# Performance work log

Hardware: AMD Instinct MI355X
Metric: run time of the kernel (lower is better)

Reference implementation:

```python
import jax, jax.numpy as jnp
import numpy as np

S_, T_, F_, SF_, G_ = 16, 400, 16, 250, 4  # systems, time, features, shuffleFactor, feature groups


def setup_inputs() -> dict:
    key = jax.random.key(0)
    ks = jax.random.split(key, 10)
    observations = jax.random.normal(ks[0], (S_, T_, F_), dtype=jnp.float32)
    mu = 0.1 * jax.random.normal(ks[1], (F_, 1), dtype=jnp.float32)
    Sigma_minus_half = (0.1 * jax.random.normal(ks[2], (F_, F_), dtype=jnp.float32)
                        + jnp.eye(F_, dtype=jnp.float32))
    # true random permutations of the time axis, per (shuffle-rep, feature-group, system)
    perm_idx = jnp.argsort(jax.random.uniform(ks[3], (SF_, G_, S_, T_)), axis=-1).astype(jnp.int32)
    W1 = jax.random.normal(ks[4], (F_, 32), dtype=jnp.float32) / jnp.sqrt(F_)
    b1 = jnp.zeros((32,), jnp.float32)
    W2 = jax.random.normal(ks[5], (32, 16), dtype=jnp.float32) / jnp.sqrt(32.0)
    b2 = jnp.zeros((16,), jnp.float32)
    W3 = jax.random.normal(ks[6], (16, 1), dtype=jnp.float32) / 4.0
    b3 = jnp.zeros((1,), jnp.float32)
    return dict(observations=observations, mu=mu, Sigma_minus_half=Sigma_minus_half,
                perm_idx=perm_idx, W1=W1, b1=b1, W2=W2, b2=b2, W3=W3, b3=b3)


def reference(observations, mu, Sigma_minus_half, perm_idx, W1, b1, W2, b2, W3, b3):
    # --- multipleShuffles: per-system, per-feature-group time permutation, repeated SF_ times ---
    feat_group = jnp.repeat(jnp.arange(G_), F_ // G_)          # [F] feature -> group id
    p = perm_idx[:, feat_group]                                 # [SF, F, S, T]
    p = jnp.transpose(p, (2, 0, 3, 1)).astype(jnp.int32)        # [S, SF, T, F]
    shuf = jnp.take_along_axis(observations[:, None, :, :], p, axis=2)  # [S, SF, T, F]
    shuf = shuf.reshape(S_, SF_ * T_, F_)                       # [S, SF*T, F]

    # --- normalizeObservations: Sigma^{-1/2} @ (z - mu) applied per (system, time) ---
    def normalize(x):
        return jnp.einsum('ij,stj->sti', Sigma_minus_half, x - mu[:, 0])

    # --- sequence MLP: Linear(F,32)-LeakyReLU-Linear(32,16)-LeakyReLU-Linear(16,1)-Sigmoid ---
    def mlp(x):
        h = jax.nn.leaky_relu(x @ W1 + b1, negative_slope=0.01)
        h = jax.nn.leaky_relu(h @ W2 + b2, negative_slope=0.01)
        return jax.nn.sigmoid(h @ W3 + b3)

    comb = mlp(normalize(observations))      # [S, T, 1]
    comb_shuf = mlp(normalize(shuf))         # [S, SF*T, 1]
    return jnp.concatenate([comb, comb_shuf], axis=1)  # [S, T*(1+SF), 1]
```

## Files before the change

### kernel.cpp

```cpp
#include <hip/hip_runtime.h>
#include <hip/hip_fp16.h>

#define S_N 16
#define T_N 400
#define F_N 16
#define SF_N 250
#define G_N 4
#define OUT_ROW 100400

typedef _Float16 f16x8 __attribute__((ext_vector_type(8)));
typedef float    f32x4 __attribute__((ext_vector_type(4)));

union QU { uint4 u; f16x8 v; };

#define QTAB_OFF   0
#define W2FRAG_OFF 1638400
#define B1H_OFF    1639424
#define B2F_OFF    1639488
#define W3F_OFF    1639552
#define B3F_OFF    1639616

#define LDS_U4     8000

__global__ __launch_bounds__(64) void precompute_kernel(
    const float* __restrict__ obs,
    const float* __restrict__ mu,
    const float* __restrict__ Sig,
    const float* __restrict__ W1,
    const float* __restrict__ b1,
    const float* __restrict__ W2,
    const float* __restrict__ b2,
    const float* __restrict__ W3,
    const float* __restrict__ b3,
    __half* __restrict__ qtab,
    __half* __restrict__ w2frag,
    __half* __restrict__ b1h,
    float* __restrict__ b2f,
    float* __restrict__ w3f,
    float* __restrict__ b3f,
    float* __restrict__ out)
{
    __shared__ float sAm[512];
    __shared__ float sW2[512];
    __shared__ float sMu[16];
    __shared__ float sB1[32];
    __shared__ float sB2[16];
    __shared__ float sW3[16];
    __shared__ float sB3;

    const int tid = threadIdx.x;

    for (int e = tid; e < 512; e += 64) {
        int j = e >> 5, k = e & 31;
        float acc = 0.f;
        #pragma unroll
        for (int i = 0; i < 16; ++i)
            acc = fmaf(Sig[i * 16 + j], W1[i * 32 + k], acc);
        sAm[e] = acc;
        sW2[e] = W2[e];
    }
    if (tid < 16) sMu[tid] = mu[tid];
    if (tid < 32) sB1[tid] = b1[tid];
    if (tid < 16) sB2[tid] = b2[tid];
    if (tid < 16) sW3[tid] = W3[tid];
    if (tid == 0) sB3 = b3[0];
    __syncthreads();

    if (blockIdx.x == 0) {
        {
            int n = tid & 15, cc = tid >> 4;
            #pragma unroll
            for (int j = 0; j < 8; ++j)
                w2frag[tid * 8 + j] = __float2half(sW2[(cc * 8 + j) * 16 + n]);
        }
        if (tid < 32) b1h[tid] = __float2half(sB1[tid]);
        if (tid < 16) b2f[tid] = sB2[tid];
        if (tid < 16) w3f[tid] = sW3[tid];
        if (tid == 0) b3f[0] = sB3;
    }

    const int gid = blockIdx.x * 64 + tid;
    const int s = gid / T_N;
    const int t = gid - s * T_N;

    float xm[16];
    {
        const float4* op = (const float4*)(obs + (size_t)gid * 16);
        float4 o0 = op[0], o1 = op[1], o2 = op[2], o3 = op[3];
        float v[16] = {o0.x, o0.y, o0.z, o0.w, o1.x, o1.y, o1.z, o1.w,
                       o2.x, o2.y, o2.z, o2.w, o3.x, o3.y, o3.z, o3.w};
        #pragma unroll
        for (int j = 0; j < 16; ++j) xm[j] = v[j] - sMu[j];
    }

    float h1[32];
    #pragma unroll
    for (int k = 0; k < 32; ++k) h1[k] = sB1[k];

    #pragma unroll
    for (int g = 0; g < 4; ++g) {
        float qg[32];
        #pragma unroll
        for (int k = 0; k < 32; ++k) {
            float a = xm[4 * g + 0] * sAm[(4 * g + 0) * 32 + k];
            a = fmaf(xm[4 * g + 1], sAm[(4 * g + 1) * 32 + k], a);
            a = fmaf(xm[4 * g + 2], sAm[(4 * g + 2) * 32 + k], a);
            a = fmaf(xm[4 * g + 3], sAm[(4 * g + 3) * 32 + k], a);
            qg[k] = a;
            h1[k] += a;
        }
        __half2* dst = (__half2*)(qtab + ((size_t)(s * 4 + g) * T_N + t) * 32);
        #pragma unroll
        for (int k2 = 0; k2 < 16; ++k2)
            dst[k2] = __floats2half2_rn(qg[2 * k2], qg[2 * k2 + 1]);
    }

    #pragma unroll
    for (int k = 0; k < 32; ++k) h1[k] = fmaxf(h1[k], 0.01f * h1[k]);

    float h2[16];
    #pragma unroll
    for (int j = 0; j < 16; ++j) h2[j] = sB2[j];
    #pragma unroll
    for (int k = 0; k < 32; ++k) {
        float a = h1[k];
        #pragma unroll
        for (int j = 0; j < 16; ++j) h2[j] = fmaf(a, sW2[k * 16 + j], h2[j]);
    }
    float acc = sB3;
    #pragma unroll
    for (int j = 0; j < 16; ++j) {
        float hj = fmaxf(h2[j], 0.01f * h2[j]);
        acc = fmaf(hj, sW3[j], acc);
    }
    out[(size_t)s * OUT_ROW + t] = 1.f / (1.f + __expf(-acc));
}

__global__ __launch_bounds__(1024, 4) void eval_kernel(
    const int* __restrict__ perm,
    const __half* __restrict__ qtab,
    const __half* __restrict__ w2frag,
    const __half* __restrict__ b1h,
    const float* __restrict__ b2f,
    const float* __restrict__ w3f,
    const float* __restrict__ b3p,
    float* __restrict__ out)
{
    extern __shared__ uint4 smem[];

    const int tid   = threadIdx.x;
    const int s     = blockIdx.x >> 4;
    const int chunk = blockIdx.x & 15;
    const int j0b   = chunk * 6250;

    const uint4* qsrc = (const uint4*)(qtab + (size_t)s * 1600 * 32);
    for (int e = tid; e < 6400; e += 1024) {
        int r = e >> 2, cc = e & 3;
        smem[r * 5 + cc] = qsrc[e];
    }
    __syncthreads();

    const int lane = tid & 63;
    const int wv   = tid >> 6;
    const int m    = lane & 15;
    const int c    = lane >> 4;

    const f16x8 afrag = *(const f16x8*)(w2frag + lane * 8);
    const f16x8 b1v   = *(const f16x8*)(b1h + c * 8);
    const float4 b2v  = *(const float4*)(b2f + c * 4);
    const float4 w3v  = *(const float4*)(w3f + c * 4);
    const float  b3   = b3p[0];

    for (int tile = wv; tile < 98; tile += 16) {
        const int jt = j0b + tile * 64;

        int idx[4][4];
        #pragma unroll
        for (int q = 0; q < 4; ++q) {
            int j = jt + q * 16 + m;
            int jc = j0b + 6249;
            if (j < jc) jc = j;
            const int sf = jc / 400;
            const int t  = jc - sf * 400;
            const int pb = sf * 25600 + s * 400 + t;
            #pragma unroll
            for (int g = 0; g < 4; ++g)
                idx[q][g] = perm[pb + g * 6400];
        }

        float res0, res1, res2, res3;
        #pragma unroll
        for (int q = 0; q < 4; ++q) {
            QU a0, a1, a2, a3;
            a0.u = smem[(idx[q][0]         ) * 5 + c];
            a1.u = smem[( 400 + idx[q][1]  ) * 5 + c];
            a2.u = smem[( 800 + idx[q][2]  ) * 5 + c];
            a3.u = smem[(1200 + idx[q][3]  ) * 5 + c];

            f16x8 h = (a0.v + a1.v) + (a2.v + a3.v) + b1v;
            #pragma unroll
            for (int k = 0; k < 8; ++k) {
                _Float16 x = h[k];
                _Float16 y = x * (_Float16)0.01f;
                h[k] = x > y ? x : y;
            }

            f32x4 acc = {0.f, 0.f, 0.f, 0.f};
            acc = __builtin_amdgcn_mfma_f32_16x16x32_f16(afrag, h, acc, 0, 0, 0);

            float p;
            {
                float v0 = acc[0] + b2v.x; v0 = fmaxf(v0, 0.01f * v0); p = v0 * w3v.x;
                float v1 = acc[1] + b2v.y; v1 = fmaxf(v1, 0.01f * v1); p = fmaf(v1, w3v.y, p);
                float v2 = acc[2] + b2v.z; v2 = fmaxf(v2, 0.01f * v2); p = fmaf(v2, w3v.z, p);
                float v3 = acc[3] + b2v.w; v3 = fmaxf(v3, 0.01f * v3); p = fmaf(v3, w3v.w, p);
            }
            p += __shfl_xor(p, 16);
            p += __shfl_xor(p, 32);
            if (q == 0) res0 = p;
            else if (q == 1) res1 = p;
            else if (q == 2) res2 = p;
            else res3 = p;
        }

        float v = res0;
        if (c == 1) v = res1;
        if (c == 2) v = res2;
        if (c == 3) v = res3;
        v += b3;
        const float sg = 1.f / (1.f + __expf(-v));
        const int j = jt + lane;
        if (j < j0b + 6250)
            out[(size_t)s * OUT_ROW + 400 + j] = sg;
    }
}

extern "C" void kernel_launch(void* const* d_in, const int* in_sizes, int n_in,
                              void* d_out, int out_size, void* d_ws, size_t ws_size,
                              hipStream_t stream) {
    (void)in_sizes; (void)n_in; (void)out_size; (void)ws_size;
    const float* obs = (const float*)d_in[0];
    const float* mu  = (const float*)d_in[1];
    const float* Sig = (const float*)d_in[2];
    const int*   prm = (const int*)d_in[3];
    const float* W1  = (const float*)d_in[4];
    const float* b1  = (const float*)d_in[5];
    const float* W2  = (const float*)d_in[6];
    const float* b2  = (const float*)d_in[7];
    const float* W3  = (const float*)d_in[8];
    const float* b3  = (const float*)d_in[9];

    char* ws = (char*)d_ws;
    __half* qtab   = (__half*)(ws + QTAB_OFF);
    __half* w2frag = (__half*)(ws + W2FRAG_OFF);
    __half* b1h    = (__half*)(ws + B1H_OFF);
    float*  b2f    = (float*)(ws + B2F_OFF);
    float*  w3f    = (float*)(ws + W3F_OFF);
    float*  b3f    = (float*)(ws + B3F_OFF);
    float*  out    = (float*)d_out;

    (void)hipFuncSetAttribute((const void*)eval_kernel,
                              hipFuncAttributeMaxDynamicSharedMemorySize,
                              LDS_U4 * 16);

    hipLaunchKernelGGL(precompute_kernel, dim3(100), dim3(64), 0, stream,
                       obs, mu, Sig, W1, b1, W2, b2, W3, b3,
                       qtab, w2frag, b1h, b2f, w3f, b3f, out);
    hipLaunchKernelGGL(eval_kernel, dim3(256), dim3(1024), LDS_U4 * 16, stream,
                       prm, qtab, w2frag, b1h, b2f, w3f, b3f, out);
}
```

Before: 117.2 us.

## Fuse precompute and eval kernels, building the per-group table directly in LDS

Merges the two kernels into one. Each block now computes its system's per-group projection table (obs minus mu, times Sigma^-1/2·W1) straight into shared memory, and computes the unshuffled outputs for its slice. This removes the second launch, the global write and readback of qtab, and the fragment staging through workspace. In exchange every block recomputes the Sigma·W1 product and its system's table, 16 times redundantly per system. The unshuffled MLP also runs on only 25 threads per block and reads fp16-rounded table values instead of fp32.

```diff
diff --git a/kernel.cpp b/kernel.cpp
--- a/kernel.cpp
+++ b/kernel.cpp
@@ -13,33 +13,23 @@
 
 union QU { uint4 u; f16x8 v; };
 
-#define QTAB_OFF   0
-#define W2FRAG_OFF 1638400
-#define B1H_OFF    1639424
-#define B2F_OFF    1639488
-#define W3F_OFF    1639552
-#define B3F_OFF    1639616
-
-#define LDS_U4     8000
-
-__global__ __launch_bounds__(64) void precompute_kernel(
+#define LDS_U4   8000
+
+__global__ __launch_bounds__(1024, 4) void fused_kernel(
     const float* __restrict__ obs,
     const float* __restrict__ mu,
     const float* __restrict__ Sig,
+    const int*   __restrict__ perm,
     const float* __restrict__ W1,
     const float* __restrict__ b1,
     const float* __restrict__ W2,
     const float* __restrict__ b2,
     const float* __restrict__ W3,
     const float* __restrict__ b3,
-    __half* __restrict__ qtab,
-    __half* __restrict__ w2frag,
-    __half* __restrict__ b1h,
-    float* __restrict__ b2f,
-    float* __restrict__ w3f,
-    float* __restrict__ b3f,
     float* __restrict__ out)
 {
+    extern __shared__ uint4 smem[];
+
     __shared__ float sAm[512];
     __shared__ float sW2[512];
     __shared__ float sMu[16];
@@ -48,16 +38,20 @@
     __shared__ float sW3[16];
     __shared__ float sB3;
 
-    const int tid = threadIdx.x;
-
-    for (int e = tid; e < 512; e += 64) {
-        int j = e >> 5, k = e & 31;
+    const int tid   = threadIdx.x;
+    const int s     = blockIdx.x >> 4;
+    const int chunk = blockIdx.x & 15;
+    const int j0b   = chunk * 6250;
+
+    if (tid < 512) {
+        const int j = tid >> 5, k = tid & 31;
         float acc = 0.f;
         #pragma unroll
         for (int i = 0; i < 16; ++i)
             acc = fmaf(Sig[i * 16 + j], W1[i * 32 + k], acc);
-        sAm[e] = acc;
-        sW2[e] = W2[e];
+        sAm[tid] = acc;
+    } else {
+        sW2[tid - 512] = W2[tid - 512];
     }
     if (tid < 16) sMu[tid] = mu[tid];
     if (tid < 32) sB1[tid] = b1[tid];
@@ -66,110 +60,81 @@
     if (tid == 0) sB3 = b3[0];
     __syncthreads();
 
-    if (blockIdx.x == 0) {
-        {
-            int n = tid & 15, cc = tid >> 4;
-            #pragma unroll
-            for (int j = 0; j < 8; ++j)
-                w2frag[tid * 8 + j] = __float2half(sW2[(cc * 8 + j) * 16 + n]);
-        }
-        if (tid < 32) b1h[tid] = __float2half(sB1[tid]);
-        if (tid < 16) b2f[tid] = sB2[tid];
-        if (tid < 16) w3f[tid] = sW3[tid];
-        if (tid == 0) b3f[0] = sB3;
-    }
-
-    const int gid = blockIdx.x * 64 + tid;
-    const int s = gid / T_N;
-    const int t = gid - s * T_N;
-
-    float xm[16];
-    {
-        const float4* op = (const float4*)(obs + (size_t)gid * 16);
-        float4 o0 = op[0], o1 = op[1], o2 = op[2], o3 = op[3];
-        float v[16] = {o0.x, o0.y, o0.z, o0.w, o1.x, o1.y, o1.z, o1.w,
-                       o2.x, o2.y, o2.z, o2.w, o3.x, o3.y, o3.z, o3.w};
-        #pragma unroll
-        for (int j = 0; j < 16; ++j) xm[j] = v[j] - sMu[j];
-    }
-
-    float h1[32];
-    #pragma unroll
-    for (int k = 0; k < 32; ++k) h1[k] = sB1[k];
-
-    #pragma unroll
-    for (int g = 0; g < 4; ++g) {
-        float qg[32];
+    for (int e = tid; e < 1600; e += 1024) {
+        const int t = e >> 2, g = e & 3;
+        const float4 o = *(const float4*)(obs + ((size_t)s * 400 + t) * 16 + g * 4);
+        const float x0 = o.x - sMu[4 * g + 0];
+        const float x1 = o.y - sMu[4 * g + 1];
+        const float x2 = o.z - sMu[4 * g + 2];
+        const float x3 = o.w - sMu[4 * g + 3];
+        const float* A0 = sAm + (4 * g + 0) * 32;
+        const float* A1 = sAm + (4 * g + 1) * 32;
+        const float* A2 = sAm + (4 * g + 2) * 32;
+        const float* A3 = sAm + (4 * g + 3) * 32;
+        uint4 row[4];
+        __half2* hp = (__half2*)row;
+        #pragma unroll
+        for (int k2 = 0; k2 < 16; ++k2) {
+            float qa = x0 * A0[2 * k2];
+            qa = fmaf(x1, A1[2 * k2], qa);
+            qa = fmaf(x2, A2[2 * k2], qa);
+            qa = fmaf(x3, A3[2 * k2], qa);
+            float qb = x0 * A0[2 * k2 + 1];
+            qb = fmaf(x1, A1[2 * k2 + 1], qb);
+            qb = fmaf(x2, A2[2 * k2 + 1], qb);
+            qb = fmaf(x3, A3[2 * k2 + 1], qb);
+            hp[k2] = __floats2half2_rn(qa, qb);
+        }
+        uint4* dst = &smem[(g * 400 + t) * 5];
+        dst[0] = row[0]; dst[1] = row[1]; dst[2] = row[2]; dst[3] = row[3];
+    }
+    __syncthreads();
+
+    if (tid < 25) {
+        const int t = chunk * 25 + tid;
+        float h1[32];
+        #pragma unroll
+        for (int k = 0; k < 32; ++k) h1[k] = sB1[k];
+        #pragma unroll
+        for (int g = 0; g < 4; ++g) {
+            const __half* qr = (const __half*)&smem[(g * 400 + t) * 5];
+            #pragma unroll
+            for (int k = 0; k < 32; ++k) h1[k] += (float)qr[k];
+        }
+        #pragma unroll
+        for (int k = 0; k < 32; ++k) h1[k] = fmaxf(h1[k], 0.01f * h1[k]);
+        float h2[16];
+        #pragma unroll
+        for (int j = 0; j < 16; ++j) h2[j] = sB2[j];
         #pragma unroll
         for (int k = 0; k < 32; ++k) {
-            float a = xm[4 * g + 0] * sAm[(4 * g + 0) * 32 + k];
-            a = fmaf(xm[4 * g + 1], sAm[(4 * g + 1) * 32 + k], a);
-            a = fmaf(xm[4 * g + 2], sAm[(4 * g + 2) * 32 + k], a);
-            a = fmaf(xm[4 * g + 3], sAm[(4 * g + 3) * 32 + k], a);
-            qg[k] = a;
-            h1[k] += a;
-        }
-        __half2* dst = (__half2*)(qtab + ((size_t)(s * 4 + g) * T_N + t) * 32);
-        #pragma unroll
-        for (int k2 = 0; k2 < 16; ++k2)
-            dst[k2] = __floats2half2_rn(qg[2 * k2], qg[2 * k2 + 1]);
-    }
-
-    #pragma unroll
-    for (int k = 0; k < 32; ++k) h1[k] = fmaxf(h1[k], 0.01f * h1[k]);
-
-    float h2[16];
-    #pragma unroll
-    for (int j = 0; j < 16; ++j) h2[j] = sB2[j];
-    #pragma unroll
-    for (int k = 0; k < 32; ++k) {
-        float a = h1[k];
-        #pragma unroll
-        for (int j = 0; j < 16; ++j) h2[j] = fmaf(a, sW2[k * 16 + j], h2[j]);
-    }
-    float acc = sB3;
-    #pragma unroll
-    for (int j = 0; j < 16; ++j) {
-        float hj = fmaxf(h2[j], 0.01f * h2[j]);
-        acc = fmaf(hj, sW3[j], acc);
-    }
-    out[(size_t)s * OUT_ROW + t] = 1.f / (1.f + __expf(-acc));
-}
-
-__global__ __launch_bounds__(1024, 4) void eval_kernel(
-    const int* __restrict__ perm,
-    const __half* __restrict__ qtab,
-    const __half* __restrict__ w2frag,
-    const __half* __restrict__ b1h,
-    const float* __restrict__ b2f,
-    const float* __restrict__ w3f,
-    const float* __restrict__ b3p,
-    float* __restrict__ out)
-{
-    extern __shared__ uint4 smem[];
-
-    const int tid   = threadIdx.x;
-    const int s     = blockIdx.x >> 4;
-    const int chunk = blockIdx.x & 15;
-    const int j0b   = chunk * 6250;
-
-    const uint4* qsrc = (const uint4*)(qtab + (size_t)s * 1600 * 32);
-    for (int e = tid; e < 6400; e += 1024) {
-        int r = e >> 2, cc = e & 3;
-        smem[r * 5 + cc] = qsrc[e];
-    }
-    __syncthreads();
+            const float a = h1[k];
+            #pragma unroll
+            for (int j = 0; j < 16; ++j) h2[j] = fmaf(a, sW2[k * 16 + j], h2[j]);
+        }
+        float acc = sB3;
+        #pragma unroll
+        for (int j = 0; j < 16; ++j) {
+            const float hj = fmaxf(h2[j], 0.01f * h2[j]);
+            acc = fmaf(hj, sW3[j], acc);
+        }
+        out[(size_t)s * OUT_ROW + t] = 1.f / (1.f + __expf(-acc));
+    }
 
     const int lane = tid & 63;
     const int wv   = tid >> 6;
     const int m    = lane & 15;
     const int c    = lane >> 4;
 
-    const f16x8 afrag = *(const f16x8*)(w2frag + lane * 8);
-    const f16x8 b1v   = *(const f16x8*)(b1h + c * 8);
-    const float4 b2v  = *(const float4*)(b2f + c * 4);
-    const float4 w3v  = *(const float4*)(w3f + c * 4);
-    const float  b3   = b3p[0];
+    f16x8 afrag, b1v;
+    #pragma unroll
+    for (int j = 0; j < 8; ++j) {
+        afrag[j] = (_Float16)sW2[(c * 8 + j) * 16 + m];
+        b1v[j]   = (_Float16)sB1[c * 8 + j];
+    }
+    const float4 b2v = *(const float4*)(sB2 + c * 4);
+    const float4 w3v = *(const float4*)(sW3 + c * 4);
+    const float  b3s = sB3;
 
     for (int tile = wv; tile < 98; tile += 16) {
         const int jt = j0b + tile * 64;
@@ -192,10 +157,10 @@
         #pragma unroll
         for (int q = 0; q < 4; ++q) {
             QU a0, a1, a2, a3;
-            a0.u = smem[(idx[q][0]         ) * 5 + c];
-            a1.u = smem[( 400 + idx[q][1]  ) * 5 + c];
-            a2.u = smem[( 800 + idx[q][2]  ) * 5 + c];
-            a3.u = smem[(1200 + idx[q][3]  ) * 5 + c];
+            a0.u = smem[(idx[q][0]        ) * 5 + c];
+            a1.u = smem[( 400 + idx[q][1] ) * 5 + c];
+            a2.u = smem[( 800 + idx[q][2] ) * 5 + c];
+            a3.u = smem[(1200 + idx[q][3] ) * 5 + c];
 
             f16x8 h = (a0.v + a1.v) + (a2.v + a3.v) + b1v;
             #pragma unroll
@@ -227,7 +192,7 @@
         if (c == 1) v = res1;
         if (c == 2) v = res2;
         if (c == 3) v = res3;
-        v += b3;
+        v += b3s;
         const float sg = 1.f / (1.f + __expf(-v));
         const int j = jt + lane;
         if (j < j0b + 6250)
@@ -238,7 +203,7 @@
 extern "C" void kernel_launch(void* const* d_in, const int* in_sizes, int n_in,
                               void* d_out, int out_size, void* d_ws, size_t ws_size,
                               hipStream_t stream) {
-    (void)in_sizes; (void)n_in; (void)out_size; (void)ws_size;
+    (void)in_sizes; (void)n_in; (void)out_size; (void)d_ws; (void)ws_size;
     const float* obs = (const float*)d_in[0];
     const float* mu  = (const float*)d_in[1];
     const float* Sig = (const float*)d_in[2];
@@ -249,23 +214,12 @@
     const float* b2  = (const float*)d_in[7];
     const float* W3  = (const float*)d_in[8];
     const float* b3  = (const float*)d_in[9];
-
-    char* ws = (char*)d_ws;
-    __half* qtab   = (__half*)(ws + QTAB_OFF);
-    __half* w2frag = (__half*)(ws + W2FRAG_OFF);
-    __half* b1h    = (__half*)(ws + B1H_OFF);
-    float*  b2f    = (float*)(ws + B2F_OFF);
-    float*  w3f    = (float*)(ws + W3F_OFF);
-    float*  b3f    = (float*)(ws + B3F_OFF);
-    float*  out    = (float*)d_out;
-
-    (void)hipFuncSetAttribute((const void*)eval_kernel,
+    float* out = (float*)d_out;
+
+    (void)hipFuncSetAttribute((const void*)fused_kernel,
                               hipFuncAttributeMaxDynamicSharedMemorySize,
                               LDS_U4 * 16);
 
-    hipLaunchKernelGGL(precompute_kernel, dim3(100), dim3(64), 0, stream,
-                       obs, mu, Sig, W1, b1, W2, b2, W3, b3,
-                       qtab, w2frag, b1h, b2f, w3f, b3f, out);
-    hipLaunchKernelGGL(eval_kernel, dim3(256), dim3(1024), LDS_U4 * 16, stream,
-                       prm, qtab, w2frag, b1h, b2f, w3f, b3f, out);
+    hipLaunchKernelGGL(fused_kernel, dim3(256), dim3(1024), LDS_U4 * 16, stream,
+                       obs, mu, Sig, prm, W1, b1, W2, b2, W3, b3, out);
 }
```

Measured after the change: 125.4 us. 1.07x slower.
